# Performance work log

Hardware: AMD Instinct MI355X
Metric: run time of the kernel (lower is better)

The kernel has to match this reference:

```python
import jax, jax.numpy as jnp
import numpy as np

TF = 1e-4  # temperature_forward (eval-mode STE uses this)
NPX = 1024
NPY = 1024
V = 16
C = 10


def setup_inputs() -> dict:
    key = jax.random.key(0)
    k1, k2, k3, k4 = jax.random.split(key, 4)
    x = jnp.linspace(0.0, 1.0, NPX, dtype=jnp.float32)
    y = jnp.linspace(0.0, 1.0, NPY, dtype=jnp.float32)
    gx, gy = jnp.meshgrid(x, y, indexing='ij')
    return {
        'split_points': jax.random.uniform(k1, (V,), jnp.float32) * 0.6 + 0.2,
        'split_directions_logits': jax.random.normal(k2, (V,), jnp.float32),
        'class_logits': jax.random.normal(k3, (V, C), jnp.float32),
        'child_selection_logits': jax.random.normal(k4, (V, 2, V), jnp.float32),
        'x_positions': gx.reshape(-1),
        'y_positions': gy.reshape(-1),
        'max_depth': 8,
    }


def _sig(x):
    return jax.nn.sigmoid(x / TF)


def reference(split_points, split_directions_logits, class_logits, child_selection_logits, x_positions, y_positions, max_depth):
    B = x_positions.shape[0]
    sp = jnp.clip(split_points, 0.1, 0.9)            # [V]
    d = jax.nn.sigmoid(split_directions_logits)       # [V]
    Cl = jax.nn.softmax(child_selection_logits[:, 0, :] / TF, axis=-1)  # [V,V]
    Cr = jax.nn.softmax(child_selection_logits[:, 1, :] / TF, axis=-1)  # [V,V]

    node_probs = jnp.zeros((B, V), x_positions.dtype).at[:, 0].set(1.0)
    min_x = jnp.zeros_like(x_positions)
    max_x = jnp.ones_like(x_positions)
    min_y = jnp.zeros_like(y_positions)
    max_y = jnp.ones_like(y_positions)

    for _ in range(max_depth):
        split_x = min_x[:, None] + sp[None, :] * (max_x - min_x)[:, None]  # [B,V]
        split_y = min_y[:, None] + sp[None, :] * (max_y - min_y)[:, None]  # [B,V]
        h_left = _sig(split_x - x_positions[:, None])
        v_left = _sig(split_y - y_positions[:, None])
        left = ((1.0 - d) * h_left + d * v_left) * node_probs   # [B,V]
        right = node_probs - left                                # node_weight*(1-p)

        next_probs = jnp.einsum('bn,nc->bc', left, Cl) + jnp.einsum('bn,nc->bc', right, Cr)

        # boxes depend only on the parent node; child probs sum to 1
        lb_max_x = (1.0 - d) * split_x + d * max_x[:, None]
        rb_min_x = (1.0 - d) * split_x + d * min_x[:, None]
        lb_max_y = d * split_y + (1.0 - d) * max_y[:, None]
        rb_min_y = d * split_y + (1.0 - d) * min_y[:, None]

        w = left + right
        weight_sum = jnp.maximum(w.sum(axis=1), 1e-10)
        next_min_x = min_x * left.sum(axis=1) + (rb_min_x * right).sum(axis=1)
        next_max_x = (lb_max_x * left).sum(axis=1) + max_x * right.sum(axis=1)
        next_min_y = min_y * left.sum(axis=1) + (rb_min_y * right).sum(axis=1)
        next_max_y = (lb_max_y * left).sum(axis=1) + max_y * right.sum(axis=1)

        node_probs = next_probs / jnp.maximum(next_probs.sum(axis=1, keepdims=True), 1e-10)
        min_x = next_min_x / weight_sum
        max_x = next_max_x / weight_sum
        min_y = next_min_y / weight_sum
        max_y = next_max_y / weight_sum

    cls = jax.nn.softmax(class_logits / TF, axis=1)  # [V,C]
    class_probs = node_probs @ cls                    # [B,C]
    return class_probs.reshape(NPX, NPY, C)
```

## Files before the change

### kernel.cpp

```cpp
#include <hip/hip_runtime.h>
#include <math.h>

#define V 16
#define NC 10
#define NPX 1024
#define NPY 1024

static constexpr float TF = 1e-4f;
static constexpr float INV_TF = 1.0f / TF;

#define WS_SP 0
#define WS_D 16
#define WS_OD 32
#define WS_CL 48
#define WS_CR 304
#define WS_CLS 560

__global__ void setup_kernel(const float* __restrict__ split_points,
                             const float* __restrict__ dir_logits,
                             const float* __restrict__ class_logits,
                             const float* __restrict__ child_logits,
                             float* __restrict__ ws) {
    const int t = threadIdx.x;
    if (t < V) {
        float s = fminf(fmaxf(split_points[t], 0.1f), 0.9f);
        ws[WS_SP + t] = s;
        float dd = 1.0f / (1.0f + expf(-dir_logits[t]));
        ws[WS_D + t] = dd;
        ws[WS_OD + t] = 1.0f - dd;
        float u[V]; float m = -INFINITY;
        #pragma unroll
        for (int c = 0; c < V; ++c) { u[c] = child_logits[t * 2 * V + c] * INV_TF; m = fmaxf(m, u[c]); }
        float sum = 0.0f;
        #pragma unroll
        for (int c = 0; c < V; ++c) { u[c] = expf(u[c] - m); sum += u[c]; }
        #pragma unroll
        for (int c = 0; c < V; ++c) ws[WS_CL + t * V + c] = u[c] / sum;
    } else if (t < 2 * V) {
        const int n = t - V;
        float u[V]; float m = -INFINITY;
        #pragma unroll
        for (int c = 0; c < V; ++c) { u[c] = child_logits[n * 2 * V + V + c] * INV_TF; m = fmaxf(m, u[c]); }
        float sum = 0.0f;
        #pragma unroll
        for (int c = 0; c < V; ++c) { u[c] = expf(u[c] - m); sum += u[c]; }
        #pragma unroll
        for (int c = 0; c < V; ++c) ws[WS_CR + n * V + c] = u[c] / sum;
    } else if (t < 3 * V) {
        const int n = t - 2 * V;
        float u[NC]; float m = -INFINITY;
        #pragma unroll
        for (int c = 0; c < NC; ++c) { u[c] = class_logits[n * NC + c] * INV_TF; m = fmaxf(m, u[c]); }
        float sum = 0.0f;
        #pragma unroll
        for (int c = 0; c < NC; ++c) { u[c] = expf(u[c] - m); sum += u[c]; }
        #pragma unroll
        for (int c = 0; c < NC; ++c) ws[WS_CLS + n * NC + c] = u[c] / sum;
    }
}

__device__ __forceinline__ float fast_sigmoid(float z) {
    return __builtin_amdgcn_rcpf(1.0f + __expf(-z));
}

__global__ __launch_bounds__(256) void fractal_kernel(
        const float* __restrict__ ws,
        const float* __restrict__ xs,
        const float* __restrict__ ys,
        const int* __restrict__ max_depth_p,
        float* __restrict__ out,
        int B) {
    const int lane = threadIdx.x & 63;
    const int wave = threadIdx.x >> 6;
    const int tile = blockIdx.x * 4 + wave;
    if (tile >= (B >> 6)) return;
    const int tx = tile >> 7;
    const int ty = tile & 127;
    const int ix = tx * 8 + (lane >> 3);
    const int iy = ty * 8 + (lane & 7);
    const int p = ix * NPY + iy;

    const float x = xs[p];
    const float y = ys[p];
    const int depth = *max_depth_p;

    float np[V];
    #pragma unroll
    for (int n = 0; n < V; ++n) np[n] = 0.0f;
    np[0] = 1.0f;
    float minx = 0.0f, maxx = 1.0f, miny = 0.0f, maxy = 1.0f;

    #pragma unroll 1
    for (int t = 0; t < depth; ++t) {
        const float rx = maxx - minx;
        const float ry = maxy - miny;
        float nxt[V];
        #pragma unroll
        for (int c = 0; c < V; ++c) nxt[c] = 0.0f;
        float sum_l = 0.0f, sum_r = 0.0f;
        float acc_lmaxx = 0.0f, acc_rminx = 0.0f;
        float acc_lmaxy = 0.0f, acc_rminy = 0.0f;

        #pragma unroll
        for (int n = 0; n < V; ++n) {
            if (__any(np[n] != 0.0f)) {
                const float spn = ws[WS_SP + n];
                const float dn  = ws[WS_D + n];
                const float odn = ws[WS_OD + n];
                const float sx = fmaf(spn, rx, minx);
                const float sy = fmaf(spn, ry, miny);
                const float h = fast_sigmoid((sx - x) * INV_TF);
                const float v = fast_sigmoid((sy - y) * INV_TF);
                const float l = fmaf(dn, v, odn * h) * np[n];
                const float r = np[n] - l;
                sum_l += l;
                sum_r += r;
                acc_lmaxx = fmaf(fmaf(dn, maxx, odn * sx), l, acc_lmaxx);
                acc_rminx = fmaf(fmaf(dn, minx, odn * sx), r, acc_rminx);
                acc_lmaxy = fmaf(fmaf(odn, maxy, dn * sy), l, acc_lmaxy);
                acc_rminy = fmaf(fmaf(odn, miny, dn * sy), r, acc_rminy);
                #pragma unroll
                for (int c = 0; c < V; ++c) {
                    nxt[c] = fmaf(l, ws[WS_CL + n * V + c],
                             fmaf(r, ws[WS_CR + n * V + c], nxt[c]));
                }
            }
        }

        float wsum = fmaxf(sum_l + sum_r, 1e-10f);
        const float inv_w = __builtin_amdgcn_rcpf(wsum);
        float psum = 0.0f;
        #pragma unroll
        for (int c = 0; c < V; ++c) psum += nxt[c];
        const float inv_p = __builtin_amdgcn_rcpf(fmaxf(psum, 1e-10f));
        #pragma unroll
        for (int c = 0; c < V; ++c) np[c] = nxt[c] * inv_p;

        const float nminx = fmaf(minx, sum_l, acc_rminx) * inv_w;
        const float nmaxx = fmaf(maxx, sum_r, acc_lmaxx) * inv_w;
        const float nminy = fmaf(miny, sum_l, acc_rminy) * inv_w;
        const float nmaxy = fmaf(maxy, sum_r, acc_lmaxy) * inv_w;
        minx = nminx; maxx = nmaxx; miny = nminy; maxy = nmaxy;
    }

    float o[NC];
    #pragma unroll
    for (int c = 0; c < NC; ++c) o[c] = 0.0f;
    #pragma unroll
    for (int n = 0; n < V; ++n) {
        if (__any(np[n] != 0.0f)) {
            #pragma unroll
            for (int c = 0; c < NC; ++c) o[c] = fmaf(np[n], ws[WS_CLS + n * NC + c], o[c]);
        }
    }

    float2* op = reinterpret_cast<float2*>(out + (size_t)p * NC);
    #pragma unroll
    for (int c = 0; c < NC / 2; ++c) op[c] = make_float2(o[2 * c], o[2 * c + 1]);
}

extern "C" void kernel_launch(void* const* d_in, const int* in_sizes, int n_in,
                              void* d_out, int out_size, void* d_ws, size_t ws_size,
                              hipStream_t stream) {
    const float* split_points = (const float*)d_in[0];
    const float* dir_logits   = (const float*)d_in[1];
    const float* class_logits = (const float*)d_in[2];
    const float* child_logits = (const float*)d_in[3];
    const float* xs           = (const float*)d_in[4];
    const float* ys           = (const float*)d_in[5];
    const int*   max_depth    = (const int*)d_in[6];
    float* out = (float*)d_out;
    float* ws  = (float*)d_ws;

    hipLaunchKernelGGL(setup_kernel, dim3(1), dim3(64), 0, stream,
                       split_points, dir_logits, class_logits, child_logits, ws);

    const int B = in_sizes[4];
    const int blocks = (B + 255) / 256;
    hipLaunchKernelGGL(fractal_kernel, dim3(blocks), dim3(256), 0, stream,
                       ws, xs, ys, max_depth, out, B);
}
```

Baseline: 153.6 us.

## Exploit one-hot child selection with LDS scatter and persistent atomic tile scheduler

The setup kernel now checks whether every row of the child-selection softmax is exactly one-hot. If so, it records each row's target index and sets a flag. When the flag is set, the main kernel replaces the dense 16x16 mixing with two LDS atomic adds per active node into per-wave accumulators, read back with atomicExch. The main kernel also becomes persistent: 2048 blocks grab 64-pixel tiles through a global atomic counter, and launch bounds now request 8 blocks per CU. This trades the per-node dense FMA work for LDS atomics and a global atomic per tile.

```diff
diff --git a/kernel.cpp b/kernel.cpp
--- a/kernel.cpp
+++ b/kernel.cpp
@@ -9,12 +9,19 @@
 static constexpr float TF = 1e-4f;
 static constexpr float INV_TF = 1.0f / TF;
 
-#define WS_SP 0
-#define WS_D 16
-#define WS_OD 32
-#define WS_CL 48
-#define WS_CR 304
-#define WS_CLS 560
+enum {
+    WS_SP   = 0,
+    WS_D    = WS_SP + 16,
+    WS_OD   = WS_D + 16,
+    WS_CL   = WS_OD + 16,
+    WS_CR   = WS_CL + 256,
+    WS_CLS  = WS_CR + 256,
+    WS_CLO  = WS_CLS + 160,
+    WS_CRO  = WS_CLO + 16,
+    WS_FLAG = WS_CRO + 16,
+    WS_CTR  = WS_FLAG + 1,
+    WS_TOTAL = WS_CTR + 1
+};
 
 __global__ void setup_kernel(const float* __restrict__ split_points,
                              const float* __restrict__ dir_logits,
@@ -22,40 +29,47 @@
                              const float* __restrict__ child_logits,
                              float* __restrict__ ws) {
     const int t = threadIdx.x;
-    if (t < V) {
+    int* wsi = (int*)ws;
+    if (t == 0) { wsi[WS_CTR] = 0; wsi[WS_FLAG] = 1; }
+    __syncthreads();
+
+    if (t < 16) {
         float s = fminf(fmaxf(split_points[t], 0.1f), 0.9f);
         ws[WS_SP + t] = s;
         float dd = 1.0f / (1.0f + expf(-dir_logits[t]));
         ws[WS_D + t] = dd;
         ws[WS_OD + t] = 1.0f - dd;
+    }
+    if (t < 32) {
+        const int n = t & (V - 1);
+        const int side = t >> 4;
+        const float* row = child_logits + n * 2 * V + side * V;
         float u[V]; float m = -INFINITY;
         #pragma unroll
-        for (int c = 0; c < V; ++c) { u[c] = child_logits[t * 2 * V + c] * INV_TF; m = fmaxf(m, u[c]); }
+        for (int c = 0; c < V; ++c) { u[c] = row[c] * INV_TF; m = fmaxf(m, u[c]); }
         float sum = 0.0f;
         #pragma unroll
         for (int c = 0; c < V; ++c) { u[c] = expf(u[c] - m); sum += u[c]; }
-        #pragma unroll
-        for (int c = 0; c < V; ++c) ws[WS_CL + t * V + c] = u[c] / sum;
-    } else if (t < 2 * V) {
-        const int n = t - V;
-        float u[V]; float m = -INFINITY;
-        #pragma unroll
-        for (int c = 0; c < V; ++c) { u[c] = child_logits[n * 2 * V + V + c] * INV_TF; m = fmaxf(m, u[c]); }
-        float sum = 0.0f;
-        #pragma unroll
-        for (int c = 0; c < V; ++c) { u[c] = expf(u[c] - m); sum += u[c]; }
-        #pragma unroll
-        for (int c = 0; c < V; ++c) ws[WS_CR + n * V + c] = u[c] / sum;
-    } else if (t < 3 * V) {
-        const int n = t - 2 * V;
-        float u[NC]; float m = -INFINITY;
-        #pragma unroll
-        for (int c = 0; c < NC; ++c) { u[c] = class_logits[n * NC + c] * INV_TF; m = fmaxf(m, u[c]); }
-        float sum = 0.0f;
-        #pragma unroll
-        for (int c = 0; c < NC; ++c) { u[c] = expf(u[c] - m); sum += u[c]; }
-        #pragma unroll
-        for (int c = 0; c < NC; ++c) ws[WS_CLS + n * NC + c] = u[c] / sum;
+        const int dense_at = (side ? WS_CR : WS_CL) + n * V;
+        int cnt = 0, idx = 0; float pv = 0.0f;
+        #pragma unroll
+        for (int c = 0; c < V; ++c) {
+            float p = u[c] / sum;
+            ws[dense_at + c] = p;
+            if (p != 0.0f) { ++cnt; idx = c; pv = p; }
+        }
+        if (cnt != 1 || pv != 1.0f) atomicAnd(&wsi[WS_FLAG], 0);
+        wsi[(side ? WS_CRO : WS_CLO) + n] = idx * 64;
+    } else if (t < 48) {
+        const int n = t - 32;
+        float uc[NC]; float mc = -INFINITY;
+        #pragma unroll
+        for (int c = 0; c < NC; ++c) { uc[c] = class_logits[n * NC + c] * INV_TF; mc = fmaxf(mc, uc[c]); }
+        float sc = 0.0f;
+        #pragma unroll
+        for (int c = 0; c < NC; ++c) { uc[c] = expf(uc[c] - mc); sc += uc[c]; }
+        #pragma unroll
+        for (int c = 0; c < NC; ++c) ws[WS_CLS + n * NC + c] = uc[c] / sc;
     }
 }
 
@@ -63,100 +77,144 @@
     return __builtin_amdgcn_rcpf(1.0f + __expf(-z));
 }
 
-__global__ __launch_bounds__(256) void fractal_kernel(
+__global__ __launch_bounds__(256, 8) void fractal_kernel(
         const float* __restrict__ ws,
+        int* __restrict__ ctr,
         const float* __restrict__ xs,
         const float* __restrict__ ys,
         const int* __restrict__ max_depth_p,
         float* __restrict__ out,
-        int B) {
+        int nt) {
+    __shared__ float acc_s[4 * V * 64];
     const int lane = threadIdx.x & 63;
     const int wave = threadIdx.x >> 6;
-    const int tile = blockIdx.x * 4 + wave;
-    if (tile >= (B >> 6)) return;
-    const int tx = tile >> 7;
-    const int ty = tile & 127;
-    const int ix = tx * 8 + (lane >> 3);
-    const int iy = ty * 8 + (lane & 7);
-    const int p = ix * NPY + iy;
-
-    const float x = xs[p];
-    const float y = ys[p];
+    float* A = acc_s + wave * (V * 64);
+    const int* wsi = (const int*)ws;
+
+    #pragma unroll
+    for (int c = 0; c < V; ++c) A[c * 64 + lane] = 0.0f;
+
     const int depth = *max_depth_p;
-
-    float np[V];
-    #pragma unroll
-    for (int n = 0; n < V; ++n) np[n] = 0.0f;
-    np[0] = 1.0f;
-    float minx = 0.0f, maxx = 1.0f, miny = 0.0f, maxy = 1.0f;
-
-    #pragma unroll 1
-    for (int t = 0; t < depth; ++t) {
-        const float rx = maxx - minx;
-        const float ry = maxy - miny;
-        float nxt[V];
-        #pragma unroll
-        for (int c = 0; c < V; ++c) nxt[c] = 0.0f;
-        float sum_l = 0.0f, sum_r = 0.0f;
-        float acc_lmaxx = 0.0f, acc_rminx = 0.0f;
-        float acc_lmaxy = 0.0f, acc_rminy = 0.0f;
-
+    const bool onehot = wsi[WS_FLAG] != 0;
+
+    for (;;) {
+        int tile;
+        if (lane == 0) tile = atomicAdd(ctr, 1);
+        tile = __shfl(tile, 0, 64);
+        if (tile >= nt) break;
+
+        const int tx = tile >> 7;
+        const int ty = tile & 127;
+        const int ix = tx * 8 + (lane >> 3);
+        const int iy = ty * 8 + (lane & 7);
+        const int p = ix * NPY + iy;
+
+        const float x = xs[p];
+        const float y = ys[p];
+
+        float np[V];
+        #pragma unroll
+        for (int n = 0; n < V; ++n) np[n] = 0.0f;
+        np[0] = 1.0f;
+        float minx = 0.0f, maxx = 1.0f, miny = 0.0f, maxy = 1.0f;
+
+        #pragma unroll 1
+        for (int t = 0; t < depth; ++t) {
+            const float rx = maxx - minx;
+            const float ry = maxy - miny;
+            float nxt[V];
+            #pragma unroll
+            for (int c = 0; c < V; ++c) nxt[c] = 0.0f;
+            float sum_l = 0.0f, sum_r = 0.0f;
+            float acc_lmaxx = 0.0f, acc_rminx = 0.0f;
+            float acc_lmaxy = 0.0f, acc_rminy = 0.0f;
+
+            if (onehot) {
+                #pragma unroll
+                for (int n = 0; n < V; ++n) {
+                    if (__any(np[n] != 0.0f)) {
+                        const float spn = ws[WS_SP + n];
+                        const float dn  = ws[WS_D + n];
+                        const float odn = ws[WS_OD + n];
+                        const float sx = fmaf(spn, rx, minx);
+                        const float sy = fmaf(spn, ry, miny);
+                        const float h = fast_sigmoid((sx - x) * INV_TF);
+                        const float v = fast_sigmoid((sy - y) * INV_TF);
+                        const float l = fmaf(dn, v, odn * h) * np[n];
+                        const float r = np[n] - l;
+                        sum_l += l;
+                        sum_r += r;
+                        acc_lmaxx = fmaf(fmaf(dn, maxx, odn * sx), l, acc_lmaxx);
+                        acc_rminx = fmaf(fmaf(dn, minx, odn * sx), r, acc_rminx);
+                        acc_lmaxy = fmaf(fmaf(odn, maxy, dn * sy), l, acc_lmaxy);
+                        acc_rminy = fmaf(fmaf(odn, miny, dn * sy), r, acc_rminy);
+                        atomicAdd(&A[wsi[WS_CRO + n] + lane], r);
+                        atomicAdd(&A[wsi[WS_CLO + n] + lane], l);
+                    }
+                }
+                #pragma unroll
+                for (int c = 0; c < V; ++c)
+                    nxt[c] = atomicExch(&A[c * 64 + lane], 0.0f);
+            } else {
+                #pragma unroll
+                for (int n = 0; n < V; ++n) {
+                    if (__any(np[n] != 0.0f)) {
+                        const float spn = ws[WS_SP + n];
+                        const float dn  = ws[WS_D + n];
+                        const float odn = ws[WS_OD + n];
+                        const float sx = fmaf(spn, rx, minx);
+                        const float sy = fmaf(spn, ry, miny);
+                        const float h = fast_sigmoid((sx - x) * INV_TF);
+                        const float v = fast_sigmoid((sy - y) * INV_TF);
+                        const float l = fmaf(dn, v, odn * h) * np[n];
+                        const float r = np[n] - l;
+                        sum_l += l;
+                        sum_r += r;
+                        acc_lmaxx = fmaf(fmaf(dn, maxx, odn * sx), l, acc_lmaxx);
+                        acc_rminx = fmaf(fmaf(dn, minx, odn * sx), r, acc_rminx);
+                        acc_lmaxy = fmaf(fmaf(odn, maxy, dn * sy), l, acc_lmaxy);
+                        acc_rminy = fmaf(fmaf(odn, miny, dn * sy), r, acc_rminy);
+                        #pragma unroll
+                        for (int c = 0; c < V; ++c) {
+                            nxt[c] = fmaf(l, ws[WS_CL + n * V + c],
+                                     fmaf(r, ws[WS_CR + n * V + c], nxt[c]));
+                        }
+                    }
+                }
+            }
+
+            float wsum = fmaxf(sum_l + sum_r, 1e-10f);
+            const float inv_w = __builtin_amdgcn_rcpf(wsum);
+            float psum = 0.0f;
+            #pragma unroll
+            for (int c = 0; c < V; ++c) psum += nxt[c];
+            const float inv_p = __builtin_amdgcn_rcpf(fmaxf(psum, 1e-10f));
+            #pragma unroll
+            for (int c = 0; c < V; ++c) np[c] = nxt[c] * inv_p;
+
+            const float nminx = fmaf(minx, sum_l, acc_rminx) * inv_w;
+            const float nmaxx = fmaf(maxx, sum_r, acc_lmaxx) * inv_w;
+            const float nminy = fmaf(miny, sum_l, acc_rminy) * inv_w;
+            const float nmaxy = fmaf(maxy, sum_r, acc_lmaxy) * inv_w;
+            minx = nminx; maxx = nmaxx; miny = nminy; maxy = nmaxy;
+        }
+
+        float o[NC];
+        #pragma unroll
+        for (int c = 0; c < NC; ++c) o[c] = 0.0f;
         #pragma unroll
         for (int n = 0; n < V; ++n) {
             if (__any(np[n] != 0.0f)) {
-                const float spn = ws[WS_SP + n];
-                const float dn  = ws[WS_D + n];
-                const float odn = ws[WS_OD + n];
-                const float sx = fmaf(spn, rx, minx);
-                const float sy = fmaf(spn, ry, miny);
-                const float h = fast_sigmoid((sx - x) * INV_TF);
-                const float v = fast_sigmoid((sy - y) * INV_TF);
-                const float l = fmaf(dn, v, odn * h) * np[n];
-                const float r = np[n] - l;
-                sum_l += l;
-                sum_r += r;
-                acc_lmaxx = fmaf(fmaf(dn, maxx, odn * sx), l, acc_lmaxx);
-                acc_rminx = fmaf(fmaf(dn, minx, odn * sx), r, acc_rminx);
-                acc_lmaxy = fmaf(fmaf(odn, maxy, dn * sy), l, acc_lmaxy);
-                acc_rminy = fmaf(fmaf(odn, miny, dn * sy), r, acc_rminy);
-                #pragma unroll
-                for (int c = 0; c < V; ++c) {
-                    nxt[c] = fmaf(l, ws[WS_CL + n * V + c],
-                             fmaf(r, ws[WS_CR + n * V + c], nxt[c]));
-                }
+                #pragma unroll
+                for (int c = 0; c < NC; ++c)
+                    o[c] = fmaf(np[n], ws[WS_CLS + n * NC + c], o[c]);
             }
         }
 
-        float wsum = fmaxf(sum_l + sum_r, 1e-10f);
-        const float inv_w = __builtin_amdgcn_rcpf(wsum);
-        float psum = 0.0f;
-        #pragma unroll
-        for (int c = 0; c < V; ++c) psum += nxt[c];
-        const float inv_p = __builtin_amdgcn_rcpf(fmaxf(psum, 1e-10f));
-        #pragma unroll
-        for (int c = 0; c < V; ++c) np[c] = nxt[c] * inv_p;
-
-        const float nminx = fmaf(minx, sum_l, acc_rminx) * inv_w;
-        const float nmaxx = fmaf(maxx, sum_r, acc_lmaxx) * inv_w;
-        const float nminy = fmaf(miny, sum_l, acc_rminy) * inv_w;
-        const float nmaxy = fmaf(maxy, sum_r, acc_lmaxy) * inv_w;
-        minx = nminx; maxx = nmaxx; miny = nminy; maxy = nmaxy;
+        float2* op = reinterpret_cast<float2*>(out + (size_t)p * NC);
+        #pragma unroll
+        for (int c = 0; c < NC / 2; ++c) op[c] = make_float2(o[2 * c], o[2 * c + 1]);
     }
-
-    float o[NC];
-    #pragma unroll
-    for (int c = 0; c < NC; ++c) o[c] = 0.0f;
-    #pragma unroll
-    for (int n = 0; n < V; ++n) {
-        if (__any(np[n] != 0.0f)) {
-            #pragma unroll
-            for (int c = 0; c < NC; ++c) o[c] = fmaf(np[n], ws[WS_CLS + n * NC + c], o[c]);
-        }
-    }
-
-    float2* op = reinterpret_cast<float2*>(out + (size_t)p * NC);
-    #pragma unroll
-    for (int c = 0; c < NC / 2; ++c) op[c] = make_float2(o[2 * c], o[2 * c + 1]);
 }
 
 extern "C" void kernel_launch(void* const* d_in, const int* in_sizes, int n_in,
@@ -171,12 +229,13 @@
     const int*   max_depth    = (const int*)d_in[6];
     float* out = (float*)d_out;
     float* ws  = (float*)d_ws;
+    int* ctr   = (int*)ws + WS_CTR;
 
     hipLaunchKernelGGL(setup_kernel, dim3(1), dim3(64), 0, stream,
                        split_points, dir_logits, class_logits, child_logits, ws);
 
     const int B = in_sizes[4];
-    const int blocks = (B + 255) / 256;
-    hipLaunchKernelGGL(fractal_kernel, dim3(blocks), dim3(256), 0, stream,
-                       ws, xs, ys, max_depth, out, B);
-}
+    const int nt = B >> 6;
+    hipLaunchKernelGGL(fractal_kernel, dim3(2048), dim3(256), 0, stream,
+                       ws, ctr, xs, ys, max_depth, out, nt);
+}
```

After: 366.4 us. 139% more time.

## Compress near-one-hot child and class softmax matrices into sparse gather lists

Applied to the files above, without the earlier changes.

The setup kernel now builds per-output-column sparse lists of nonzero entries from the child-selection and class softmax matrices, together with the maximum nonzero count. The main kernel stages the left and right probabilities for each wave in LDS. It then accumulates next-level probabilities and class outputs by gathering only those nonzero entries, replacing the dense V×V FMAs. The goal is to exploit the near one-hot softmax at tiny temperature to cut arithmetic, at the cost of LDS writes and reads. Launch bounds also now request higher occupancy.

```diff
diff --git a/kernel.cpp b/kernel.cpp
--- a/kernel.cpp
+++ b/kernel.cpp
@@ -9,53 +9,98 @@
 static constexpr float TF = 1e-4f;
 static constexpr float INV_TF = 1.0f / TF;
 
-#define WS_SP 0
-#define WS_D 16
-#define WS_OD 32
-#define WS_CL 48
-#define WS_CR 304
-#define WS_CLS 560
+enum {
+    WS_SP   = 0,
+    WS_D    = WS_SP + 16,
+    WS_OD   = WS_D + 16,
+    WS_MOFF = WS_OD + 16,
+    WS_MVAL = WS_MOFF + 256,
+    WS_COFF = WS_MVAL + 256,
+    WS_CVAL = WS_COFF + 256,
+    WS_K    = WS_CVAL + 256,
+    WS_K2   = WS_K + 1,
+    WS_TOTAL = WS_K2 + 1
+};
 
 __global__ void setup_kernel(const float* __restrict__ split_points,
                              const float* __restrict__ dir_logits,
                              const float* __restrict__ class_logits,
                              const float* __restrict__ child_logits,
                              float* __restrict__ ws) {
+    __shared__ float P[2][V][V];
+    __shared__ float CL[V][NC];
+    __shared__ int cnt_mix[V];
+    __shared__ int cnt_cls[NC];
     const int t = threadIdx.x;
+    int* wsi = (int*)ws;
+
     if (t < V) {
         float s = fminf(fmaxf(split_points[t], 0.1f), 0.9f);
         ws[WS_SP + t] = s;
         float dd = 1.0f / (1.0f + expf(-dir_logits[t]));
         ws[WS_D + t] = dd;
         ws[WS_OD + t] = 1.0f - dd;
+    }
+    if (t < 2 * V) {
+        const int n = t & (V - 1);
+        const int side = t >> 4;
+        const float* row = child_logits + n * 2 * V + side * V;
         float u[V]; float m = -INFINITY;
         #pragma unroll
-        for (int c = 0; c < V; ++c) { u[c] = child_logits[t * 2 * V + c] * INV_TF; m = fmaxf(m, u[c]); }
+        for (int c = 0; c < V; ++c) { u[c] = row[c] * INV_TF; m = fmaxf(m, u[c]); }
         float sum = 0.0f;
         #pragma unroll
         for (int c = 0; c < V; ++c) { u[c] = expf(u[c] - m); sum += u[c]; }
         #pragma unroll
-        for (int c = 0; c < V; ++c) ws[WS_CL + t * V + c] = u[c] / sum;
-    } else if (t < 2 * V) {
-        const int n = t - V;
-        float u[V]; float m = -INFINITY;
-        #pragma unroll
-        for (int c = 0; c < V; ++c) { u[c] = child_logits[n * 2 * V + V + c] * INV_TF; m = fmaxf(m, u[c]); }
-        float sum = 0.0f;
-        #pragma unroll
-        for (int c = 0; c < V; ++c) { u[c] = expf(u[c] - m); sum += u[c]; }
-        #pragma unroll
-        for (int c = 0; c < V; ++c) ws[WS_CR + n * V + c] = u[c] / sum;
+        for (int c = 0; c < V; ++c) P[side][n][c] = u[c] / sum;
     } else if (t < 3 * V) {
         const int n = t - 2 * V;
-        float u[NC]; float m = -INFINITY;
-        #pragma unroll
-        for (int c = 0; c < NC; ++c) { u[c] = class_logits[n * NC + c] * INV_TF; m = fmaxf(m, u[c]); }
-        float sum = 0.0f;
-        #pragma unroll
-        for (int c = 0; c < NC; ++c) { u[c] = expf(u[c] - m); sum += u[c]; }
-        #pragma unroll
-        for (int c = 0; c < NC; ++c) ws[WS_CLS + n * NC + c] = u[c] / sum;
+        float uc[NC]; float mc = -INFINITY;
+        #pragma unroll
+        for (int c = 0; c < NC; ++c) { uc[c] = class_logits[n * NC + c] * INV_TF; mc = fmaxf(mc, uc[c]); }
+        float sc = 0.0f;
+        #pragma unroll
+        for (int c = 0; c < NC; ++c) { uc[c] = expf(uc[c] - mc); sc += uc[c]; }
+        #pragma unroll
+        for (int c = 0; c < NC; ++c) CL[n][c] = uc[c] / sc;
+    }
+    __syncthreads();
+
+    if (t < V) {
+        int cnt = 0;
+        for (int n = 0; n < V; ++n) {
+            float vr = P[1][n][t];
+            if (vr != 0.0f) { wsi[WS_MOFF + cnt * 16 + t] = n * 64;        ws[WS_MVAL + cnt * 16 + t] = vr; ++cnt; }
+            float vl = P[0][n][t];
+            if (vl != 0.0f) { wsi[WS_MOFF + cnt * 16 + t] = 1024 + n * 64; ws[WS_MVAL + cnt * 16 + t] = vl; ++cnt; }
+        }
+        cnt_mix[t] = cnt;
+        for (int k = cnt; k < 16; ++k) {
+            wsi[WS_MOFF + k * 16 + t] = 0;
+            ws[WS_MVAL + k * 16 + t] = 0.0f;
+        }
+    }
+    if (t >= V && t < V + NC) {
+        const int c = t - V;
+        int cnt = 0;
+        for (int n = 0; n < V; ++n) {
+            float v = CL[n][c];
+            if (v != 0.0f) { wsi[WS_COFF + cnt * 16 + c] = n * 64; ws[WS_CVAL + cnt * 16 + c] = v; ++cnt; }
+        }
+        cnt_cls[c] = cnt;
+        for (int k = cnt; k < 16; ++k) {
+            wsi[WS_COFF + k * 16 + c] = 0;
+            ws[WS_CVAL + k * 16 + c] = 0.0f;
+        }
+    }
+    __syncthreads();
+    if (t == 0) {
+        int K = 0;
+        for (int c = 0; c < V; ++c) K = max(K, cnt_mix[c]);
+        wsi[WS_K] = K;
+        int K2 = 0;
+        for (int c = 0; c < NC; ++c) K2 = max(K2, cnt_cls[c]);
+        wsi[WS_K2] = K2;
     }
 }
 
@@ -63,17 +108,21 @@
     return __builtin_amdgcn_rcpf(1.0f + __expf(-z));
 }
 
-__global__ __launch_bounds__(256) void fractal_kernel(
+__global__ __launch_bounds__(256, 5) void fractal_kernel(
         const float* __restrict__ ws,
         const float* __restrict__ xs,
         const float* __restrict__ ys,
         const int* __restrict__ max_depth_p,
         float* __restrict__ out,
-        int B) {
+        int nt) {
+    __shared__ float lds[4 * 2048];
     const int lane = threadIdx.x & 63;
     const int wave = threadIdx.x >> 6;
+    float* AR = lds + wave * 2048;
+    const int* wsi = (const int*)ws;
+
     const int tile = blockIdx.x * 4 + wave;
-    if (tile >= (B >> 6)) return;
+    if (tile >= nt) return;
     const int tx = tile >> 7;
     const int ty = tile & 127;
     const int ix = tx * 8 + (lane >> 3);
@@ -83,6 +132,8 @@
     const float x = xs[p];
     const float y = ys[p];
     const int depth = *max_depth_p;
+    const int K  = wsi[WS_K];
+    const int K2 = wsi[WS_K2];
 
     float np[V];
     #pragma unroll
@@ -94,9 +145,6 @@
     for (int t = 0; t < depth; ++t) {
         const float rx = maxx - minx;
         const float ry = maxy - miny;
-        float nxt[V];
-        #pragma unroll
-        for (int c = 0; c < V; ++c) nxt[c] = 0.0f;
         float sum_l = 0.0f, sum_r = 0.0f;
         float acc_lmaxx = 0.0f, acc_rminx = 0.0f;
         float acc_lmaxy = 0.0f, acc_rminy = 0.0f;
@@ -119,11 +167,23 @@
                 acc_rminx = fmaf(fmaf(dn, minx, odn * sx), r, acc_rminx);
                 acc_lmaxy = fmaf(fmaf(odn, maxy, dn * sy), l, acc_lmaxy);
                 acc_rminy = fmaf(fmaf(odn, miny, dn * sy), r, acc_rminy);
-                #pragma unroll
-                for (int c = 0; c < V; ++c) {
-                    nxt[c] = fmaf(l, ws[WS_CL + n * V + c],
-                             fmaf(r, ws[WS_CR + n * V + c], nxt[c]));
-                }
+                AR[n * 64 + lane] = r;
+                AR[1024 + n * 64 + lane] = l;
+            } else {
+                AR[n * 64 + lane] = 0.0f;
+                AR[1024 + n * 64 + lane] = 0.0f;
+            }
+        }
+
+        float nxt[V];
+        #pragma unroll
+        for (int c = 0; c < V; ++c) nxt[c] = 0.0f;
+        for (int k = 0; k < K; ++k) {
+            #pragma unroll
+            for (int c = 0; c < V; ++c) {
+                const int off  = wsi[WS_MOFF + k * 16 + c];
+                const float vv = ws[WS_MVAL + k * 16 + c];
+                nxt[c] = fmaf(AR[off + lane], vv, nxt[c]);
             }
         }
 
@@ -143,14 +203,18 @@
         minx = nminx; maxx = nmaxx; miny = nminy; maxy = nmaxy;
     }
 
+    #pragma unroll
+    for (int n = 0; n < V; ++n) AR[n * 64 + lane] = np[n];
+
     float o[NC];
     #pragma unroll
     for (int c = 0; c < NC; ++c) o[c] = 0.0f;
-    #pragma unroll
-    for (int n = 0; n < V; ++n) {
-        if (__any(np[n] != 0.0f)) {
-            #pragma unroll
-            for (int c = 0; c < NC; ++c) o[c] = fmaf(np[n], ws[WS_CLS + n * NC + c], o[c]);
+    for (int k = 0; k < K2; ++k) {
+        #pragma unroll
+        for (int c = 0; c < NC; ++c) {
+            const int off  = wsi[WS_COFF + k * 16 + c];
+            const float vv = ws[WS_CVAL + k * 16 + c];
+            o[c] = fmaf(AR[off + lane], vv, o[c]);
         }
     }
 
@@ -176,7 +240,7 @@
                        split_points, dir_logits, class_logits, child_logits, ws);
 
     const int B = in_sizes[4];
-    const int blocks = (B + 255) / 256;
-    hipLaunchKernelGGL(fractal_kernel, dim3(blocks), dim3(256), 0, stream,
-                       ws, xs, ys, max_depth, out, B);
-}
+    const int nt = B >> 6;
+    hipLaunchKernelGGL(fractal_kernel, dim3(nt / 4), dim3(256), 0, stream,
+                       ws, xs, ys, max_depth, out, nt);
+}
```

Result: slower. 192.0 us (+25.0%).

## Scatter sparse child-selection weights into per-wave LDS accumulators

Applied to the files above, without the earlier changes.

Setup now compresses each row of the child-selection softmax matrices into a sparse list of nonzero children and their weights. The main kernel stops doing a dense 16x16 FMA per active node and instead adds l and r into per-lane LDS slots (one lane per column, a padded stride per wave) for only the nonzero children, then reads and clears those slots at each depth. This aims to cut ALU work and constant loads, since with a tiny temperature the softmax rows are nearly one-hot. The cost is LDS atomic traffic, a variable-length inner loop and extra LDS reads and writes per step.

```diff
diff --git a/kernel.cpp b/kernel.cpp
--- a/kernel.cpp
+++ b/kernel.cpp
@@ -9,12 +9,19 @@
 static constexpr float TF = 1e-4f;
 static constexpr float INV_TF = 1.0f / TF;
 
-#define WS_SP 0
-#define WS_D 16
-#define WS_OD 32
-#define WS_CL 48
-#define WS_CR 304
-#define WS_CLS 560
+enum {
+    WS_SP  = 0,
+    WS_D   = 16,
+    WS_OD  = 32,
+    WS_CLS = 48,
+    WS_CNL = 208,
+    WS_CNR = 224,
+    WS_CHL = 240,
+    WS_CHR = 496,
+    WS_VLL = 752,
+    WS_VLR = 1008,
+    WS_TOTAL = 1264
+};
 
 __global__ void setup_kernel(const float* __restrict__ split_points,
                              const float* __restrict__ dir_logits,
@@ -22,30 +29,37 @@
                              const float* __restrict__ child_logits,
                              float* __restrict__ ws) {
     const int t = threadIdx.x;
+    int* wsi = (int*)ws;
     if (t < V) {
         float s = fminf(fmaxf(split_points[t], 0.1f), 0.9f);
         ws[WS_SP + t] = s;
         float dd = 1.0f / (1.0f + expf(-dir_logits[t]));
         ws[WS_D + t] = dd;
         ws[WS_OD + t] = 1.0f - dd;
+    }
+    if (t < 2 * V) {
+        const int n = t & (V - 1);
+        const int side = t >> 4;
+        const float* row = child_logits + n * 2 * V + side * V;
         float u[V]; float m = -INFINITY;
         #pragma unroll
-        for (int c = 0; c < V; ++c) { u[c] = child_logits[t * 2 * V + c] * INV_TF; m = fmaxf(m, u[c]); }
+        for (int c = 0; c < V; ++c) { u[c] = row[c] * INV_TF; m = fmaxf(m, u[c]); }
         float sum = 0.0f;
         #pragma unroll
         for (int c = 0; c < V; ++c) { u[c] = expf(u[c] - m); sum += u[c]; }
-        #pragma unroll
-        for (int c = 0; c < V; ++c) ws[WS_CL + t * V + c] = u[c] / sum;
-    } else if (t < 2 * V) {
-        const int n = t - V;
-        float u[V]; float m = -INFINITY;
-        #pragma unroll
-        for (int c = 0; c < V; ++c) { u[c] = child_logits[n * 2 * V + V + c] * INV_TF; m = fmaxf(m, u[c]); }
-        float sum = 0.0f;
-        #pragma unroll
-        for (int c = 0; c < V; ++c) { u[c] = expf(u[c] - m); sum += u[c]; }
-        #pragma unroll
-        for (int c = 0; c < V; ++c) ws[WS_CR + n * V + c] = u[c] / sum;
+        int cnt = 0;
+        const int ch_at = (side ? WS_CHR : WS_CHL) + n * 16;
+        const int vl_at = (side ? WS_VLR : WS_VLL) + n * 16;
+        #pragma unroll
+        for (int c = 0; c < V; ++c) {
+            float p = u[c] / sum;
+            if (p != 0.0f) {
+                wsi[ch_at + cnt] = c;
+                ws[vl_at + cnt] = p;
+                ++cnt;
+            }
+        }
+        wsi[(side ? WS_CNR : WS_CNL) + n] = cnt;
     } else if (t < 3 * V) {
         const int n = t - 2 * V;
         float u[NC]; float m = -INFINITY;
@@ -62,6 +76,8 @@
 __device__ __forceinline__ float fast_sigmoid(float z) {
     return __builtin_amdgcn_rcpf(1.0f + __expf(-z));
 }
+
+#define SLOT_STRIDE 66
 
 __global__ __launch_bounds__(256) void fractal_kernel(
         const float* __restrict__ ws,
@@ -70,8 +86,11 @@
         const int* __restrict__ max_depth_p,
         float* __restrict__ out,
         int B) {
+    __shared__ float lds[4 * V * SLOT_STRIDE];
     const int lane = threadIdx.x & 63;
     const int wave = threadIdx.x >> 6;
+    float* A = lds + wave * (V * SLOT_STRIDE);
+
     const int tile = blockIdx.x * 4 + wave;
     if (tile >= (B >> 6)) return;
     const int tx = tile >> 7;
@@ -83,6 +102,17 @@
     const float x = xs[p];
     const float y = ys[p];
     const int depth = *max_depth_p;
+    const int* wsi = (const int*)ws;
+
+    #pragma unroll
+    for (int c = 0; c < V; ++c) A[c * SLOT_STRIDE + lane] = 0.0f;
+
+    int idxL0[V], idxR0[V];
+    #pragma unroll
+    for (int n = 0; n < V; ++n) {
+        idxL0[n] = wsi[WS_CHL + n * 16] * SLOT_STRIDE + lane;
+        idxR0[n] = wsi[WS_CHR + n * 16] * SLOT_STRIDE + lane;
+    }
 
     float np[V];
     #pragma unroll
@@ -94,9 +124,6 @@
     for (int t = 0; t < depth; ++t) {
         const float rx = maxx - minx;
         const float ry = maxy - miny;
-        float nxt[V];
-        #pragma unroll
-        for (int c = 0; c < V; ++c) nxt[c] = 0.0f;
         float sum_l = 0.0f, sum_r = 0.0f;
         float acc_lmaxx = 0.0f, acc_rminx = 0.0f;
         float acc_lmaxy = 0.0f, acc_rminy = 0.0f;
@@ -119,13 +146,30 @@
                 acc_rminx = fmaf(fmaf(dn, minx, odn * sx), r, acc_rminx);
                 acc_lmaxy = fmaf(fmaf(odn, maxy, dn * sy), l, acc_lmaxy);
                 acc_rminy = fmaf(fmaf(odn, miny, dn * sy), r, acc_rminy);
-                #pragma unroll
-                for (int c = 0; c < V; ++c) {
-                    nxt[c] = fmaf(l, ws[WS_CL + n * V + c],
-                             fmaf(r, ws[WS_CR + n * V + c], nxt[c]));
+                atomicAdd(&A[idxR0[n]], r * ws[WS_VLR + n * 16]);
+                const int cnr = wsi[WS_CNR + n];
+                if (cnr > 1) {
+                    for (int k = 1; k < cnr; ++k)
+                        atomicAdd(&A[wsi[WS_CHR + n * 16 + k] * SLOT_STRIDE + lane],
+                                  r * ws[WS_VLR + n * 16 + k]);
+                }
+                atomicAdd(&A[idxL0[n]], l * ws[WS_VLL + n * 16]);
+                const int cnl = wsi[WS_CNL + n];
+                if (cnl > 1) {
+                    for (int k = 1; k < cnl; ++k)
+                        atomicAdd(&A[wsi[WS_CHL + n * 16 + k] * SLOT_STRIDE + lane],
+                                  l * ws[WS_VLL + n * 16 + k]);
                 }
             }
         }
+
+        asm volatile("" ::: "memory");
+        float nxt[V];
+        #pragma unroll
+        for (int c = 0; c < V; ++c) nxt[c] = A[c * SLOT_STRIDE + lane];
+        #pragma unroll
+        for (int c = 0; c < V; ++c) A[c * SLOT_STRIDE + lane] = 0.0f;
+        asm volatile("" ::: "memory");
 
         float wsum = fmaxf(sum_l + sum_r, 1e-10f);
         const float inv_w = __builtin_amdgcn_rcpf(wsum);
```

Result: slower. 599.0 us (+290.0%).
